# Performance work log

Hardware: AMD Instinct MI355X
Metric: run time of the kernel (lower is better)

The kernel has to match this reference:

```python
import jax, jax.numpy as jnp
import numpy as np

B, T, D, H = 8192, 2048, 2, 2


def setup_inputs() -> dict:
    key = jax.random.key(0)
    ks = jax.random.split(key, 7)
    return {
        "x": jax.random.normal(ks[0], (B, T, D), dtype=jnp.float32),
        "h0": jax.random.normal(ks[1], (B, H), dtype=jnp.float32),
        "c0": jax.random.normal(ks[2], (B, H), dtype=jnp.float32),
        "w_ih": jax.random.normal(ks[3], (4 * H, D), dtype=jnp.float32),
        "w_hh": jax.random.normal(ks[4], (4 * H, H), dtype=jnp.float32),
        "b_ih": jax.random.normal(ks[5], (4 * H,), dtype=jnp.float32),
        "b_hh": jax.random.normal(ks[6], (4 * H,), dtype=jnp.float32),
    }


def reference(x, h0, c0, w_ih, w_hh, b_ih, b_hh):
    # Precompute input projections for all timesteps in one GEMM: (T, B, 4H)
    xg = jnp.einsum("btd,gd->tbg", x, w_ih) + b_ih

    def step(carry, xt_g):
        h, c = carry
        gates = xt_g + h @ w_hh.T + b_hh  # (B, 4H)
        i, f, g, o = jnp.split(gates, 4, axis=-1)  # torch lstm_cell gate order: i,f,g,o
        c = jax.nn.sigmoid(f) * c + jax.nn.sigmoid(i) * jnp.tanh(g)
        h = jax.nn.sigmoid(o) * jnp.tanh(c)
        return (h, c), None

    (h, c), _ = jax.lax.scan(step, (h0, c0), xg)
    return c
```

## Files before the change

kernel.cpp:

```cpp
#include <hip/hip_runtime.h>


#define LOG2E 1.4426950408889634f

template <int CTRL>
__device__ __forceinline__ float qperm(float v) {
    int i = __builtin_bit_cast(int, v);
    i = __builtin_amdgcn_update_dpp(0, i, CTRL, 0xf, 0xf, true);
    return __builtin_bit_cast(float, i);
}
#define QP_BCAST0 0x00
#define QP_BCAST1 0x55
#define QP_SWAP2  0x4E

__device__ __forceinline__ float tanh_f(float x) {
    return 1.0f - 2.0f * __builtin_amdgcn_rcpf(1.0f + __builtin_amdgcn_exp2f((2.0f * LOG2E) * x));
}

__global__ __launch_bounds__(64, 1) void lstm_quad_db_kernel(
    const float* __restrict__ x,
    const float* __restrict__ h0,
    const float* __restrict__ c0,
    const float* __restrict__ w_ih,
    const float* __restrict__ w_hh,
    const float* __restrict__ b_ih,
    const float* __restrict__ b_hh,
    float* __restrict__ out,
    int B, int T)
{
    const int tid = blockIdx.x * blockDim.x + threadIdx.x;
    const int e = tid >> 2;
    const int q = tid & 3;
    if (e >= B) return;

    const int rA = (q < 2) ? q : q + 2;
    const int rB = rA + 2;

    const float wiA0 = w_ih[2 * rA], wiA1 = w_ih[2 * rA + 1];
    const float whA0 = w_hh[2 * rA], whA1 = w_hh[2 * rA + 1];
    const float biasA = b_ih[rA] + b_hh[rA];
    const float wiB0 = w_ih[2 * rB], wiB1 = w_ih[2 * rB + 1];
    const float whB0 = w_hh[2 * rB], whB1 = w_hh[2 * rB + 1];
    const float biasB = b_ih[rB] + b_hh[rB];

    const bool isTanh = (q >= 2);
    const float aA = isTanh ? (2.0f * LOG2E) : (-LOG2E);
    const float mA = isTanh ? -2.0f : 1.0f;
    const float dA = isTanh ? 1.0f : 0.0f;

    float h = h0[2 * e + (q & 1)];
    float c = c0[2 * e + (q & 1)];

    const int NI = T >> 1;
    const float4* __restrict__ xp =
        reinterpret_cast<const float4*>(x) + (size_t)e * NI;

    auto step = [&](float x0, float x1) {
        float hh0 = qperm<QP_BCAST0>(h);
        float hh1 = qperm<QP_BCAST1>(h);
        float axA = fmaf(wiA1, x1, fmaf(wiA0, x0, biasA));
        float axB = fmaf(wiB1, x1, fmaf(wiB0, x0, biasB));
        float gA = fmaf(whA1, hh1, fmaf(whA0, hh0, axA));
        float gB = fmaf(whB1, hh1, fmaf(whB0, hh0, axB));
        float nA = fmaf(mA, __builtin_amdgcn_rcpf(1.0f + __builtin_amdgcn_exp2f(aA * gA)), dA);
        float nB = __builtin_amdgcn_rcpf(1.0f + __builtin_amdgcn_exp2f(-LOG2E * gB));
        float xA = qperm<QP_SWAP2>(nA);
        float xB = qperm<QP_SWAP2>(nB);
        c = fmaf(nB, c, nA * xA);
        float tc = tanh_f(c);
        h = xB * tc;
    };

    constexpr int BV = 8;
    float4 A[BV], Bb[BV];

    auto loadbuf = [&](float4* buf, int batch) {
#pragma unroll
        for (int j = 0; j < BV; ++j) buf[j] = xp[batch * BV + j];
    };
    auto consume = [&](const float4* buf) {
#pragma unroll
        for (int j = 0; j < BV; ++j) {
            step(buf[j].x, buf[j].y);
            step(buf[j].z, buf[j].w);
        }
    };

    const int nb = NI / BV;
    int bi = 0;
    if (nb >= 2) {
        loadbuf(A, 0);
        loadbuf(Bb, 1);
        for (bi = 0; bi + 1 < nb; bi += 2) {
            consume(A);
            if (bi + 2 < nb) loadbuf(A, bi + 2);
            consume(Bb);
            if (bi + 3 < nb) loadbuf(Bb, bi + 3);
        }
        if (bi < nb) { consume(A); ++bi; }
    }
    for (int i = bi * BV; i < NI; ++i) {
        float4 v = xp[i];
        step(v.x, v.y);
        step(v.z, v.w);
    }

    if (q < 2) out[2 * e + q] = c;
}

extern "C" void kernel_launch(void* const* d_in, const int* in_sizes, int n_in,
                              void* d_out, int out_size, void* d_ws, size_t ws_size,
                              hipStream_t stream) {
    const float* x    = (const float*)d_in[0];
    const float* h0   = (const float*)d_in[1];
    const float* c0   = (const float*)d_in[2];
    const float* w_ih = (const float*)d_in[3];
    const float* w_hh = (const float*)d_in[4];
    const float* b_ih = (const float*)d_in[5];
    const float* b_hh = (const float*)d_in[6];
    float* out = (float*)d_out;

    const int B = in_sizes[1] / 2;
    const int T = in_sizes[0] / (B * 2);

    const int threads = B * 4;
    dim3 block(64);
    dim3 grid((threads + 63) / 64);
    hipLaunchKernelGGL(lstm_quad_db_kernel, grid, block, 0, stream,
                       x, h0, c0, w_ih, w_hh, b_ih, b_hh, out, B, T);
}
```

Baseline: 329.4 us.

## Process two batch elements per quad to interleave independent recurrence chains

Each 4-lane quad now advances two independent LSTM sequences, interleaving their steps so the serial dependency chain of one can overlap with the other. The grid is halved, and prefetch buffers are split per sequence with a smaller per-batch depth. This trades thread-level parallelism (fewer waves per CU) for instruction-level parallelism within each wave, and raises register pressure. It assumes B is even.

```diff
diff --git a/kernel.cpp b/kernel.cpp
--- a/kernel.cpp
+++ b/kernel.cpp
@@ -13,11 +13,7 @@
 #define QP_BCAST1 0x55
 #define QP_SWAP2  0x4E
 
-__device__ __forceinline__ float tanh_f(float x) {
-    return 1.0f - 2.0f * __builtin_amdgcn_rcpf(1.0f + __builtin_amdgcn_exp2f((2.0f * LOG2E) * x));
-}
-
-__global__ __launch_bounds__(64, 1) void lstm_quad_db_kernel(
+__global__ __launch_bounds__(64, 1) void lstm_quad_ilp2_kernel(
     const float* __restrict__ x,
     const float* __restrict__ h0,
     const float* __restrict__ c0,
@@ -29,9 +25,11 @@
     int B, int T)
 {
     const int tid = blockIdx.x * blockDim.x + threadIdx.x;
-    const int e = tid >> 2;
+    const int p = tid >> 2;
     const int q = tid & 3;
-    if (e >= B) return;
+    if (p >= B / 2) return;
+    const int e0 = 2 * p;
+    const int e1 = 2 * p + 1;
 
     const int rA = (q < 2) ? q : q + 2;
     const int rB = rA + 2;
@@ -48,14 +46,16 @@
     const float mA = isTanh ? -2.0f : 1.0f;
     const float dA = isTanh ? 1.0f : 0.0f;
 
-    float h = h0[2 * e + (q & 1)];
-    float c = c0[2 * e + (q & 1)];
+    float hU = h0[2 * e0 + (q & 1)], cU = c0[2 * e0 + (q & 1)];
+    float hV = h0[2 * e1 + (q & 1)], cV = c0[2 * e1 + (q & 1)];
 
     const int NI = T >> 1;
-    const float4* __restrict__ xp =
-        reinterpret_cast<const float4*>(x) + (size_t)e * NI;
+    const float4* __restrict__ xpU =
+        reinterpret_cast<const float4*>(x) + (size_t)e0 * NI;
+    const float4* __restrict__ xpV =
+        reinterpret_cast<const float4*>(x) + (size_t)e1 * NI;
 
-    auto step = [&](float x0, float x1) {
+    auto step = [&](float& h, float& c, float x0, float x1) {
         float hh0 = qperm<QP_BCAST0>(h);
         float hh1 = qperm<QP_BCAST1>(h);
         float axA = fmaf(wiA1, x1, fmaf(wiA0, x0, biasA));
@@ -67,45 +67,56 @@
         float xA = qperm<QP_SWAP2>(nA);
         float xB = qperm<QP_SWAP2>(nB);
         c = fmaf(nB, c, nA * xA);
-        float tc = tanh_f(c);
+        float tc = 1.0f - 2.0f * __builtin_amdgcn_rcpf(1.0f + __builtin_amdgcn_exp2f((2.0f * LOG2E) * c));
         h = xB * tc;
     };
 
-    constexpr int BV = 8;
-    float4 A[BV], Bb[BV];
+    constexpr int BV = 4;
+    float4 AU[BV], AV[BV], BU[BV], BVv[BV];
 
-    auto loadbuf = [&](float4* buf, int batch) {
+    auto loadU = [&](float4* buf, int batch) {
 #pragma unroll
-        for (int j = 0; j < BV; ++j) buf[j] = xp[batch * BV + j];
+        for (int j = 0; j < BV; ++j) buf[j] = xpU[batch * BV + j];
     };
-    auto consume = [&](const float4* buf) {
+    auto loadV = [&](float4* buf, int batch) {
+#pragma unroll
+        for (int j = 0; j < BV; ++j) buf[j] = xpV[batch * BV + j];
+    };
+    auto consume = [&](const float4* bu, const float4* bv) {
 #pragma unroll
         for (int j = 0; j < BV; ++j) {
-            step(buf[j].x, buf[j].y);
-            step(buf[j].z, buf[j].w);
+            step(hU, cU, bu[j].x, bu[j].y);
+            step(hV, cV, bv[j].x, bv[j].y);
+            step(hU, cU, bu[j].z, bu[j].w);
+            step(hV, cV, bv[j].z, bv[j].w);
         }
     };
 
     const int nb = NI / BV;
     int bi = 0;
     if (nb >= 2) {
-        loadbuf(A, 0);
-        loadbuf(Bb, 1);
+        loadU(AU, 0); loadV(AV, 0);
+        loadU(BU, 1); loadV(BVv, 1);
         for (bi = 0; bi + 1 < nb; bi += 2) {
-            consume(A);
-            if (bi + 2 < nb) loadbuf(A, bi + 2);
-            consume(Bb);
-            if (bi + 3 < nb) loadbuf(Bb, bi + 3);
+            consume(AU, AV);
+            if (bi + 2 < nb) { loadU(AU, bi + 2); loadV(AV, bi + 2); }
+            consume(BU, BVv);
+            if (bi + 3 < nb) { loadU(BU, bi + 3); loadV(BVv, bi + 3); }
         }
-        if (bi < nb) { consume(A); ++bi; }
+        if (bi < nb) { consume(AU, AV); ++bi; }
     }
     for (int i = bi * BV; i < NI; ++i) {
-        float4 v = xp[i];
-        step(v.x, v.y);
-        step(v.z, v.w);
+        float4 u = xpU[i], v = xpV[i];
+        step(hU, cU, u.x, u.y);
+        step(hV, cV, v.x, v.y);
+        step(hU, cU, u.z, u.w);
+        step(hV, cV, v.z, v.w);
     }
 
-    if (q < 2) out[2 * e + q] = c;
+    if (q < 2) {
+        out[2 * e0 + q] = cU;
+        out[2 * e1 + q] = cV;
+    }
 }
 
 extern "C" void kernel_launch(void* const* d_in, const int* in_sizes, int n_in,
@@ -123,9 +134,9 @@
     const int B = in_sizes[1] / 2;
     const int T = in_sizes[0] / (B * 2);
 
-    const int threads = B * 4;
+    const int threads = (B / 2) * 4;
     dim3 block(64);
     dim3 grid((threads + 63) / 64);
-    hipLaunchKernelGGL(lstm_quad_db_kernel, grid, block, 0, stream,
+    hipLaunchKernelGGL(lstm_quad_ilp2_kernel, grid, block, 0, stream,
                        x, h0, c0, w_ih, w_hh, b_ih, b_hh, out, B, T);
 }
```

After: 459.3 us. 39.4% more time.

## Split each LSTM batch element across eight lanes with DPP gate exchange

Applied to the files above, without the earlier changes.

Each batch element now uses eight lanes instead of four, so every lane computes a single gate row and does one transcendental sigmoid or tanh per step instead of two. Gate results and cell products are exchanged with DPP permutes (row half-mirror, broadcast, swap). Weights, bias and the cell state are pre-scaled by log2(e) factors to drop multiplies from the serial chain, and the cell state is scaled back at output. This shortens the per-step dependency chain and doubles the thread count, at the cost of extra permutes and selects, twice as many lanes redundantly loading the same x stream, and more wavefronts.

```diff
diff --git a/kernel.cpp b/kernel.cpp
--- a/kernel.cpp
+++ b/kernel.cpp
@@ -4,20 +4,18 @@
 #define LOG2E 1.4426950408889634f
 
 template <int CTRL>
-__device__ __forceinline__ float qperm(float v) {
+__device__ __forceinline__ float qdpp(float v) {
     int i = __builtin_bit_cast(int, v);
     i = __builtin_amdgcn_update_dpp(0, i, CTRL, 0xf, 0xf, true);
     return __builtin_bit_cast(float, i);
 }
-#define QP_BCAST0 0x00
-#define QP_BCAST1 0x55
-#define QP_SWAP2  0x4E
+#define DPP_HSEL        0x14
+#define DPP_BCAST2      0xAA
+#define DPP_BCAST3      0xFF
+#define DPP_SWAP2       0x4E
+#define DPP_HALF_MIRROR 0x141
 
-__device__ __forceinline__ float tanh_f(float x) {
-    return 1.0f - 2.0f * __builtin_amdgcn_rcpf(1.0f + __builtin_amdgcn_exp2f((2.0f * LOG2E) * x));
-}
-
-__global__ __launch_bounds__(64, 1) void lstm_quad_db_kernel(
+__global__ __launch_bounds__(64, 1) void lstm_oct_kernel(
     const float* __restrict__ x,
     const float* __restrict__ h0,
     const float* __restrict__ c0,
@@ -29,46 +27,49 @@
     int B, int T)
 {
     const int tid = blockIdx.x * blockDim.x + threadIdx.x;
-    const int e = tid >> 2;
-    const int q = tid & 3;
+    const int e = tid >> 3;
+    const int q = tid & 7;
     if (e >= B) return;
 
-    const int rA = (q < 2) ? q : q + 2;
-    const int rB = rA + 2;
+    const int r = (q < 4) ? q : 11 - q;
+    const bool isTanh = (q >= 6);
+    const bool inQ1   = (q >= 4);
+    const bool sel45  = (q == 4) || (q == 5);
+    const bool selMid = (q >= 2) && (q <= 5);
 
-    const float wiA0 = w_ih[2 * rA], wiA1 = w_ih[2 * rA + 1];
-    const float whA0 = w_hh[2 * rA], whA1 = w_hh[2 * rA + 1];
-    const float biasA = b_ih[rA] + b_hh[rA];
-    const float wiB0 = w_ih[2 * rB], wiB1 = w_ih[2 * rB + 1];
-    const float whB0 = w_hh[2 * rB], whB1 = w_hh[2 * rB + 1];
-    const float biasB = b_ih[rB] + b_hh[rB];
+    const float a = isTanh ? (2.0f * LOG2E) : (-LOG2E);
+    const float m = isTanh ? (-4.0f * LOG2E) : 1.0f;
+    const float d = isTanh ? (2.0f * LOG2E) : 0.0f;
 
-    const bool isTanh = (q >= 2);
-    const float aA = isTanh ? (2.0f * LOG2E) : (-LOG2E);
-    const float mA = isTanh ? -2.0f : 1.0f;
-    const float dA = isTanh ? 1.0f : 0.0f;
+    const float wi0 = w_ih[2 * r] * a, wi1 = w_ih[2 * r + 1] * a;
+    const float wh0 = w_hh[2 * r] * a, wh1 = w_hh[2 * r + 1] * a;
+    const float bias = (b_ih[r] + b_hh[r]) * a;
 
-    float h = h0[2 * e + (q & 1)];
-    float c = c0[2 * e + (q & 1)];
+    const int col = (q & 1) ^ ((q >> 2) & 1);
+    float h = h0[2 * e + col];
+    float c = c0[2 * e + col] * (2.0f * LOG2E);
 
     const int NI = T >> 1;
     const float4* __restrict__ xp =
         reinterpret_cast<const float4*>(x) + (size_t)e * NI;
 
     auto step = [&](float x0, float x1) {
-        float hh0 = qperm<QP_BCAST0>(h);
-        float hh1 = qperm<QP_BCAST1>(h);
-        float axA = fmaf(wiA1, x1, fmaf(wiA0, x0, biasA));
-        float axB = fmaf(wiB1, x1, fmaf(wiB0, x0, biasB));
-        float gA = fmaf(whA1, hh1, fmaf(whA0, hh0, axA));
-        float gB = fmaf(whB1, hh1, fmaf(whB0, hh0, axB));
-        float nA = fmaf(mA, __builtin_amdgcn_rcpf(1.0f + __builtin_amdgcn_exp2f(aA * gA)), dA);
-        float nB = __builtin_amdgcn_rcpf(1.0f + __builtin_amdgcn_exp2f(-LOG2E * gB));
-        float xA = qperm<QP_SWAP2>(nA);
-        float xB = qperm<QP_SWAP2>(nB);
-        c = fmaf(nB, c, nA * xA);
-        float tc = tanh_f(c);
-        h = xB * tc;
+        float hm  = qdpp<DPP_HSEL>(h);
+        float hs  = inQ1 ? hm : h;
+        float hh0 = qdpp<DPP_BCAST2>(hs);
+        float hh1 = qdpp<DPP_BCAST3>(hs);
+        float ax = fmaf(wi1, x1, fmaf(wi0, x0, bias));
+        float g  = fmaf(wh1, hh1, fmaf(wh0, hh0, ax));
+        float n  = fmaf(m, __builtin_amdgcn_rcpf(1.0f + __builtin_amdgcn_exp2f(g)), d);
+        float mv = qdpp<DPP_HALF_MIRROR>(n);
+        float X = sel45  ? mv : n;
+        float Y = selMid ? c  : mv;
+        float p = X * Y;
+        float ps = qdpp<DPP_SWAP2>(p);
+        c = p + ps;
+        float tc = fmaf(-2.0f, __builtin_amdgcn_rcpf(1.0f + __builtin_amdgcn_exp2f(c)), 1.0f);
+        float Z = sel45 ? n : mv;
+        h = Z * tc;
     };
 
     constexpr int BV = 8;
@@ -105,7 +106,7 @@
         step(v.z, v.w);
     }
 
-    if (q < 2) out[2 * e + q] = c;
+    if (q < 2) out[2 * e + q] = c * (0.5f / LOG2E);
 }
 
 extern "C" void kernel_launch(void* const* d_in, const int* in_sizes, int n_in,
@@ -123,9 +124,9 @@
     const int B = in_sizes[1] / 2;
     const int T = in_sizes[0] / (B * 2);
 
-    const int threads = B * 4;
+    const int threads = B * 8;
     dim3 block(64);
     dim3 grid((threads + 63) / 64);
-    hipLaunchKernelGGL(lstm_quad_db_kernel, grid, block, 0, stream,
+    hipLaunchKernelGGL(lstm_oct_kernel, grid, block, 0, stream,
                        x, h0, c0, w_ih, w_hh, b_ih, b_hh, out, B, T);
 }
```

Result: no change. 323.7 us (-1.7%).
